# Performance work log

Measured on AMD Instinct MI355X. Metric: run time of the kernel, lower is better.

The kernel has to match this reference:

```python
import jax, jax.numpy as jnp
import numpy as np

N_NODES = 100000
N_EDGES = 1200000
D_IN = 64
D_HID = 64
BN_EPS = 1e-5


def setup_inputs() -> dict:
    key = jax.random.key(0)
    ks = jax.random.split(key, 16)
    x = jax.random.normal(ks[0], (N_NODES, D_IN), dtype=jnp.float32)
    edge_index = jax.random.randint(ks[1], (2, N_EDGES), 0, N_NODES, dtype=jnp.int64)
    s = 1.0 / np.sqrt(D_HID)
    W1 = jax.random.uniform(ks[2], (D_IN, D_HID), jnp.float32, -s, s)
    b1 = jax.random.uniform(ks[3], (D_HID,), jnp.float32, -s, s)
    W2 = jax.random.uniform(ks[4], (D_HID, D_HID), jnp.float32, -s, s)
    b2 = jax.random.uniform(ks[5], (D_HID,), jnp.float32, -s, s)
    W3 = jax.random.uniform(ks[6], (D_HID, D_HID), jnp.float32, -s, s)
    b3 = jax.random.uniform(ks[7], (D_HID,), jnp.float32, -s, s)
    gamma1 = jnp.ones((D_HID,), jnp.float32)
    beta1 = jnp.zeros((D_HID,), jnp.float32)
    gamma2 = jnp.ones((D_HID,), jnp.float32)
    beta2 = jnp.zeros((D_HID,), jnp.float32)
    return {"x": x, "edge_index": edge_index, "batch_size": 1,
            "W1": W1, "b1": b1, "gamma1": gamma1, "beta1": beta1,
            "W2": W2, "b2": b2, "gamma2": gamma2, "beta2": beta2,
            "W3": W3, "b3": b3}


def _gcn_norm(edge_index, n):
    # PyG GCNConv: add self-loops, symmetric normalization D^-1/2 (A+I) D^-1/2
    loop = jnp.arange(n, dtype=edge_index.dtype)
    src = jnp.concatenate([edge_index[0], loop])
    dst = jnp.concatenate([edge_index[1], loop])
    deg = jax.ops.segment_sum(jnp.ones_like(dst, dtype=jnp.float32), dst, num_segments=n)
    dinv = jnp.where(deg > 0, jax.lax.rsqrt(jnp.maximum(deg, 1.0)), 0.0)
    norm = dinv[src] * dinv[dst]  # [E + N]
    return src, dst, norm


def _gcn_conv(h, W, b, src, dst, norm, n):
    h = h @ W                      # [N, D]
    msg = h[src] * norm[:, None]   # gather + scale, [E+N, D]
    out = jax.ops.segment_sum(msg, dst, num_segments=n)  # scatter-add
    return out + b


def _bn_train(h, gamma, beta):
    # BatchNorm1d over nodes, training-mode (biased batch statistics)
    m = h.mean(axis=0)
    v = h.var(axis=0)
    return (h - m) * jax.lax.rsqrt(v + BN_EPS) * gamma + beta


def reference(x, edge_index, batch_size,
              W1, b1, gamma1, beta1, W2, b2, gamma2, beta2, W3, b3):
    n = x.shape[0]
    src, dst, norm = _gcn_norm(edge_index, n)
    h = _gcn_conv(x, W1, b1, src, dst, norm, n)
    h = jax.nn.relu(_bn_train(h, gamma1, beta1))
    h = _gcn_conv(h, W2, b2, src, dst, norm, n)
    h = jax.nn.relu(_bn_train(h, gamma2, beta2))
    h = _gcn_conv(h, W3, b3, src, dst, norm, n)
    return h  # output_type == 'hidden'
```

## Files before the change

### kernel.cpp

```cpp
#include <hip/hip_runtime.h>
#include <hip/hip_bf16.h>

#define D 64

typedef __attribute__((ext_vector_type(8))) short bf16x8;
typedef __attribute__((ext_vector_type(8))) unsigned short u16x8;
typedef __attribute__((ext_vector_type(4))) float f32x4;

__device__ __forceinline__ short f2bf(float x) {
    unsigned u = __float_as_uint(x);
    unsigned r = (u + 0x7fffu + ((u >> 16) & 1u)) >> 16;
    return (short)r;
}
__device__ __forceinline__ float bf2f(unsigned short u) {
    return __uint_as_float((unsigned)u << 16);
}

__global__ void detect_kernel(const unsigned int* e32, int* flag) {
    __shared__ int nz;
    if (threadIdx.x == 0) nz = 0;
    __syncthreads();
    if (e32[2 * threadIdx.x + 1] != 0) nz = 1;
    __syncthreads();
    if (threadIdx.x == 0) *flag = (nz == 0) ? 1 : 0;
}

__device__ __forceinline__ int load_idx(const void* e, int is64, long long i) {
    if (is64) return (int)((const long long*)e)[i];
    return ((const int*)e)[i];
}

#define NBLK 256

__global__ __launch_bounds__(256) void bucket_count_kernel(
    const void* edges, const int* flag, int* pbh, int E, int shift) {
    __shared__ int h[512];
    for (int i = threadIdx.x; i < 512; i += 256) h[i] = 0;
    __syncthreads();
    int is64 = *flag;
    int chunk = (E + gridDim.x - 1) / gridDim.x;
    int s0 = blockIdx.x * chunk;
    int s1 = min(E, s0 + chunk);
    for (int e = s0 + (int)threadIdx.x; e < s1; e += 256) {
        int d = load_idx(edges, is64, (long long)E + e);
        atomicAdd(&h[d >> shift], 1);
    }
    __syncthreads();
    for (int i = threadIdx.x; i < 512; i += 256) pbh[blockIdx.x * 512 + i] = h[i];
}

__global__ __launch_bounds__(256) void colscan_kernel(int* pbh, int* btot) {
    int b = blockIdx.x;
    int k = threadIdx.x;
    __shared__ int sA[256], sB[256];
    int v = pbh[k * 512 + b];
    sA[k] = v;
    __syncthreads();
    int* src = sA;
    int* dst = sB;
    for (int d = 1; d < 256; d <<= 1) {
        dst[k] = src[k] + (k >= d ? src[k - d] : 0);
        __syncthreads();
        int* t = src; src = dst; dst = t;
    }
    pbh[k * 512 + b] = src[k] - v;
    if (k == 255) btot[b] = src[255];
}

__global__ __launch_bounds__(512) void basescan_kernel(const int* btot, int* bbase, int E) {
    __shared__ int sA[512], sB[512];
    int b = threadIdx.x;
    int v = btot[b];
    sA[b] = v;
    __syncthreads();
    int* src = sA;
    int* dst = sB;
    for (int d = 1; d < 512; d <<= 1) {
        dst[b] = src[b] + (b >= d ? src[b - d] : 0);
        __syncthreads();
        int* t = src; src = dst; dst = t;
    }
    bbase[b] = src[b] - v;
    if (b == 0) bbase[512] = E;
}

__global__ __launch_bounds__(256) void bucket_scatter_kernel(
    const void* edges, const int* flag, const int* pbh, const int* bbase,
    unsigned* staging, int E, int shift) {
    __shared__ int cur[512];
    for (int i = threadIdx.x; i < 512; i += 256)
        cur[i] = pbh[blockIdx.x * 512 + i] + bbase[i];
    __syncthreads();
    int is64 = *flag;
    int chunk = (E + gridDim.x - 1) / gridDim.x;
    int s0 = blockIdx.x * chunk;
    int s1 = min(E, s0 + chunk);
    unsigned mask = (unsigned)((1 << shift) - 1);
    for (int e = s0 + (int)threadIdx.x; e < s1; e += 256) {
        int s = load_idx(edges, is64, e);
        int d = load_idx(edges, is64, (long long)E + e);
        int b = d >> shift;
        int pos = atomicAdd(&cur[b], 1);
        staging[pos] = ((unsigned)s << shift) | ((unsigned)d & mask);
    }
}

__global__ __launch_bounds__(256) void bucket_fill_kernel(
    const unsigned* __restrict__ staging, const int* __restrict__ bbase,
    int* __restrict__ offs, float* __restrict__ dinv, int* __restrict__ srcs,
    int shift, int n, int E) {
    int b = blockIdx.x;
    int bstart = bbase[b], bend = bbase[b + 1];
    int bsz = 1 << shift;
    unsigned mask = (unsigned)(bsz - 1);
    int v0 = b << shift;
    int nloc = min(bsz, n - v0);

    __shared__ int cnt[512], cur[512], sA[512], sB[512];
    for (int i = threadIdx.x; i < bsz; i += 256) cnt[i] = 0;
    __syncthreads();
    for (int idx = bstart + (int)threadIdx.x; idx < bend; idx += 256)
        atomicAdd(&cnt[staging[idx] & mask], 1);
    __syncthreads();
    for (int i = threadIdx.x; i < bsz; i += 256) sA[i] = cnt[i];
    __syncthreads();
    int* src = sA;
    int* dst = sB;
    for (int d = 1; d < bsz; d <<= 1) {
        for (int i = threadIdx.x; i < bsz; i += 256)
            dst[i] = src[i] + (i >= d ? src[i - d] : 0);
        __syncthreads();
        int* t = src; src = dst; dst = t;
    }
    for (int i = threadIdx.x; i < bsz; i += 256) {
        int excl = src[i] - cnt[i];
        cur[i] = excl;
        if (i < nloc) {
            offs[v0 + i] = bstart + excl;
            dinv[v0 + i] = rsqrtf((float)(cnt[i] + 1));
        }
    }
    if (b == 0 && threadIdx.x == 0) offs[n] = E;
    __syncthreads();
    for (int idx = bstart + (int)threadIdx.x; idx < bend; idx += 256) {
        unsigned u = staging[idx];
        int ld = (int)(u & mask);
        int pos = atomicAdd(&cur[ld], 1);
        srcs[bstart + pos] = (int)(u >> shift);
    }
}

__global__ __launch_bounds__(256) void mm_bn_kernel(
    const float* __restrict__ Xf, const unsigned short* __restrict__ Xb, int x_is_bf16,
    const float* __restrict__ W,
    const float* __restrict__ slabs, const float* __restrict__ gamma,
    const float* __restrict__ beta, int use_bn, float inv_n,
    const float* __restrict__ dinv,
    unsigned short* __restrict__ Y, int n) {
    int lane = threadIdx.x & 63;
    int m = lane & 15;
    int quad = lane >> 4;

    __shared__ float cn[128];
    if (use_bn) {
        if (threadIdx.x < 128) {
            float s = 0.f;
#pragma unroll
            for (int k = 0; k < 16; k++) s += slabs[k * 128 + (int)threadIdx.x];
            cn[threadIdx.x] = s;
        }
        __syncthreads();
    }

    float sc[16], sh[16];
#pragma unroll
    for (int s = 0; s < 2; s++) {
#pragma unroll
        for (int j = 0; j < 8; j++) {
            float scale = 1.f, shift = 0.f;
            if (use_bn) {
                int f = s * 32 + quad * 8 + j;
                float mean = cn[f] * inv_n;
                float var = cn[64 + f] * inv_n - mean * mean;
                float rs = rsqrtf(var + 1e-5f);
                scale = rs * gamma[f];
                shift = beta[f] - mean * scale;
            }
            sc[s * 8 + j] = scale;
            sh[s * 8 + j] = shift;
        }
    }

    bf16x8 bfrag[4][2];
#pragma unroll
    for (int nt = 0; nt < 4; nt++) {
#pragma unroll
        for (int s = 0; s < 2; s++) {
#pragma unroll
            for (int j = 0; j < 8; j++) {
                int k = s * 32 + quad * 8 + j;
                bfrag[nt][s][j] = f2bf(W[k * 64 + nt * 16 + m]);
            }
        }
    }

    int wave = blockIdx.x * 4 + (threadIdx.x >> 6);
    int nwaves = gridDim.x * 4;
    int ntiles = (n + 15) >> 4;
    const f32x4 zero = {0.f, 0.f, 0.f, 0.f};

    for (int t = wave; t < ntiles; t += nwaves) {
        int r = t * 16 + m;
        if (r >= n) r = n - 1;
        float av[16];
        if (x_is_bf16) {
            const unsigned short* xr = Xb + (long long)r * 64;
            u16x8 u0 = *(const u16x8*)(xr + quad * 8);
            u16x8 u1 = *(const u16x8*)(xr + 32 + quad * 8);
#pragma unroll
            for (int j = 0; j < 8; j++) {
                av[j] = bf2f(u0[j]);
                av[8 + j] = bf2f(u1[j]);
            }
        } else {
            const float* xr = Xf + (long long)r * 64;
            f32x4 a0 = *(const f32x4*)(xr + quad * 8);
            f32x4 a1 = *(const f32x4*)(xr + quad * 8 + 4);
            f32x4 a2 = *(const f32x4*)(xr + 32 + quad * 8);
            f32x4 a3 = *(const f32x4*)(xr + 32 + quad * 8 + 4);
#pragma unroll
            for (int j = 0; j < 4; j++) {
                av[j] = a0[j];
                av[4 + j] = a1[j];
                av[8 + j] = a2[j];
                av[12 + j] = a3[j];
            }
        }
        bf16x8 A0, A1;
#pragma unroll
        for (int j = 0; j < 8; j++) {
            float v0 = av[j] * sc[j] + sh[j];
            float v1 = av[8 + j] * sc[8 + j] + sh[8 + j];
            if (use_bn) {
                v0 = fmaxf(v0, 0.f);
                v1 = fmaxf(v1, 0.f);
            }
            A0[j] = f2bf(v0);
            A1[j] = f2bf(v1);
        }

        f32x4 acc[4];
#pragma unroll
        for (int nt = 0; nt < 4; nt++) {
            acc[nt] = __builtin_amdgcn_mfma_f32_16x16x32_bf16(A0, bfrag[nt][0], zero, 0, 0, 0);
            acc[nt] = __builtin_amdgcn_mfma_f32_16x16x32_bf16(A1, bfrag[nt][1], acc[nt], 0, 0, 0);
        }

        int row0 = t * 16 + quad * 4;
        float dv[4];
#pragma unroll
        for (int i = 0; i < 4; i++) {
            int rr = row0 + i;
            dv[i] = (rr < n) ? dinv[rr] : 0.f;
        }
#pragma unroll
        for (int nt = 0; nt < 4; nt++) {
#pragma unroll
            for (int i = 0; i < 4; i++) {
                int rr = row0 + i;
                if (rr < n)
                    Y[(long long)rr * 64 + nt * 16 + m] = (unsigned short)f2bf(acc[nt][i] * dv[i]);
            }
        }
    }
}

__global__ __launch_bounds__(256) void agg_kernel(const unsigned short* __restrict__ T,
                                                  const int* __restrict__ offs,
                                                  const int* __restrict__ srcs,
                                                  const float* __restrict__ dinv,
                                                  const float* __restrict__ bias,
                                                  unsigned short* __restrict__ out16,
                                                  float* __restrict__ out32, int out_bf16,
                                                  float* __restrict__ slabs, int do_stats,
                                                  int n) {
    int v = blockIdx.x * 4 + (threadIdx.x >> 6);
    int lane = threadIdx.x & 63;
    int valid = v < n;
    int vc = valid ? v : n - 1;
    float val;
    {
        float acc = bf2f(T[((unsigned)vc << 6) + lane]);
        int j0 = __builtin_amdgcn_readfirstlane(offs[vc]);
        int j1 = __builtin_amdgcn_readfirstlane(offs[vc + 1]);
        for (int j = j0; j < j1; j += 16) {
            int sidx[16];
#pragma unroll
            for (int u = 0; u < 16; u++) {
                int jj = j + u;
                int s = srcs[jj];
                sidx[u] = (jj < j1) ? s : n;
            }
            float t[16];
#pragma unroll
            for (int u = 0; u < 16; u++)
                t[u] = bf2f(T[((unsigned)sidx[u] << 6) + lane]);
            float p0 = (t[0] + t[1]) + (t[2] + t[3]);
            float p1 = (t[4] + t[5]) + (t[6] + t[7]);
            float p2 = (t[8] + t[9]) + (t[10] + t[11]);
            float p3 = (t[12] + t[13]) + (t[14] + t[15]);
            acc += (p0 + p1) + (p2 + p3);
        }
        val = dinv[vc] * acc + bias[lane];
        if (valid) {
            if (out_bf16)
                out16[((unsigned)v << 6) + lane] = (unsigned short)f2bf(val);
            else
                out32[((unsigned)v << 6) + lane] = val;
        }
    }
    if (do_stats) {
        __shared__ float ls[256], lq[256];
        float x = valid ? val : 0.f;
        ls[threadIdx.x] = x;
        lq[threadIdx.x] = x * x;
        __syncthreads();
        int tid = threadIdx.x;
        if (tid < 128) {
            int f = tid & 63;
            const float* a = (tid < 64) ? ls : lq;
            float r = a[f] + a[64 + f] + a[128 + f] + a[192 + f];
            atomicAdd(&slabs[((unsigned)(blockIdx.x & 15)) * 128 + tid], r);
        }
    }
}

extern "C" void kernel_launch(void* const* d_in, const int* in_sizes, int n_in,
                              void* d_out, int out_size, void* d_ws, size_t ws_size,
                              hipStream_t stream) {
    const float* x = (const float*)d_in[0];
    const void* edges = d_in[1];
    const float* W1 = (const float*)d_in[3];
    const float* b1 = (const float*)d_in[4];
    const float* gamma1 = (const float*)d_in[5];
    const float* beta1 = (const float*)d_in[6];
    const float* W2 = (const float*)d_in[7];
    const float* b2 = (const float*)d_in[8];
    const float* gamma2 = (const float*)d_in[9];
    const float* beta2 = (const float*)d_in[10];
    const float* W3 = (const float*)d_in[11];
    const float* b3 = (const float*)d_in[12];

    const int N = in_sizes[0] / D;
    const int E = in_sizes[1] / 2;
    const float inv_n = 1.f / (float)N;

    int shift = 8;
    while ((((long long)N - 1) >> shift) + 1 > 512) shift++;
    const int nbuk = (int)(((long long)N - 1) >> shift) + 1;

    char* ws = (char*)d_ws;
    size_t off = 0;
    auto alloc = [&](size_t bytes) -> void* {
        void* p = ws + off;
        off = (off + bytes + 255) & ~(size_t)255;
        return p;
    };
    float*    dinv    = (float*)   alloc((size_t)N * 4);
    int*      offs    = (int*)     alloc((size_t)(N + 1) * 4);
    int*      srcs    = (int*)     alloc(((size_t)E + 16) * 4);
    unsigned* staging = (unsigned*)alloc((size_t)E * 4);
    int*      pbh     = (int*)     alloc((size_t)NBLK * 512 * 4);
    int*      btot    = (int*)     alloc(512 * 4);
    int*      bbase   = (int*)     alloc(513 * 4);
    int*      flag    = (int*)     alloc(4);
    float*    slabs   = (float*)   alloc((size_t)2 * 16 * 128 * 4);
    unsigned short* bufA = (unsigned short*)alloc((size_t)(N + 1) * D * 2);
    unsigned short* hbuf = (unsigned short*)alloc((size_t)N * D * 2);
    float*    outf    = (float*)d_out;

    const int AGGB = (N + 3) / 4;
    const int MMB  = 782;

    detect_kernel<<<1, 256, 0, stream>>>((const unsigned int*)edges, flag);
    bucket_count_kernel<<<NBLK, 256, 0, stream>>>(edges, flag, pbh, E, shift);
    colscan_kernel<<<512, 256, 0, stream>>>(pbh, btot);
    basescan_kernel<<<1, 512, 0, stream>>>(btot, bbase, E);
    bucket_scatter_kernel<<<NBLK, 256, 0, stream>>>(edges, flag, pbh, bbase, staging, E, shift);
    bucket_fill_kernel<<<nbuk, 256, 0, stream>>>(staging, bbase, offs, dinv, srcs, shift, N, E);
    hipMemsetAsync(slabs, 0, (size_t)2 * 16 * 128 * 4, stream);
    hipMemsetAsync(bufA + (size_t)N * D, 0, D * 2, stream);

    mm_bn_kernel<<<MMB, 256, 0, stream>>>(x, nullptr, 0, W1, nullptr, nullptr, nullptr, 0,
                                          inv_n, dinv, bufA, N);
    agg_kernel<<<AGGB, 256, 0, stream>>>(bufA, offs, srcs, dinv, b1, hbuf, nullptr, 1,
                                         slabs, 1, N);

    mm_bn_kernel<<<MMB, 256, 0, stream>>>(nullptr, hbuf, 1, W2, slabs, gamma1, beta1, 1,
                                          inv_n, dinv, bufA, N);
    agg_kernel<<<AGGB, 256, 0, stream>>>(bufA, offs, srcs, dinv, b2, hbuf, nullptr, 1,
                                         slabs + 16 * 128, 1, N);

    mm_bn_kernel<<<MMB, 256, 0, stream>>>(nullptr, hbuf, 1, W3, slabs + 16 * 128, gamma2, beta2, 1,
                                          inv_n, dinv, bufA, N);
    agg_kernel<<<AGGB, 256, 0, stream>>>(bufA, offs, srcs, dinv, b3, nullptr, outf, 0,
                                         nullptr, 0, N);
}
```

Measured before the change: 306.6 us.

## Fold detect and memsets into kernels, coalesce mm output via LDS, resize grid

Removes the separate detect kernel and two memset launches by detecting 64-bit edge indices inside each bucket kernel and zeroing the stats slabs and padding row from existing kernels. The matmul epilogue now stages bf16 results in shared memory and writes each row with 16-byte vector stores instead of scattered 2-byte stores. The matmul grid is sized to one tile per wave rather than a fixed block count. This trades a few extra global reads per block for fewer launches and better-coalesced writes.

New measurement: 299.8 us. 2.2% less time.

```diff
diff --git a/kernel.cpp b/kernel.cpp
--- a/kernel.cpp
+++ b/kernel.cpp
@@ -16,13 +16,13 @@
     return __uint_as_float((unsigned)u << 16);
 }
 
-__global__ void detect_kernel(const unsigned int* e32, int* flag) {
+__device__ __forceinline__ int block_detect_is64(const unsigned* e32) {
     __shared__ int nz;
     if (threadIdx.x == 0) nz = 0;
     __syncthreads();
-    if (e32[2 * threadIdx.x + 1] != 0) nz = 1;
-    __syncthreads();
-    if (threadIdx.x == 0) *flag = (nz == 0) ? 1 : 0;
+    if (threadIdx.x < 256 && e32[2 * threadIdx.x + 1] != 0) nz = 1;
+    __syncthreads();
+    return nz == 0;
 }
 
 __device__ __forceinline__ int load_idx(const void* e, int is64, long long i) {
@@ -33,11 +33,13 @@
 #define NBLK 256
 
 __global__ __launch_bounds__(256) void bucket_count_kernel(
-    const void* edges, const int* flag, int* pbh, int E, int shift) {
+    const void* edges, int* pbh, float* slabs, int E, int shift) {
+    int is64 = block_detect_is64((const unsigned*)edges);
+    if (blockIdx.x == 0)
+        for (int i = threadIdx.x; i < 2 * 16 * 128; i += 256) slabs[i] = 0.f;
     __shared__ int h[512];
     for (int i = threadIdx.x; i < 512; i += 256) h[i] = 0;
     __syncthreads();
-    int is64 = *flag;
     int chunk = (E + gridDim.x - 1) / gridDim.x;
     int s0 = blockIdx.x * chunk;
     int s1 = min(E, s0 + chunk);
@@ -85,13 +87,13 @@
 }
 
 __global__ __launch_bounds__(256) void bucket_scatter_kernel(
-    const void* edges, const int* flag, const int* pbh, const int* bbase,
+    const void* edges, const int* pbh, const int* bbase,
     unsigned* staging, int E, int shift) {
+    int is64 = block_detect_is64((const unsigned*)edges);
     __shared__ int cur[512];
     for (int i = threadIdx.x; i < 512; i += 256)
         cur[i] = pbh[blockIdx.x * 512 + i] + bbase[i];
     __syncthreads();
-    int is64 = *flag;
     int chunk = (E + gridDim.x - 1) / gridDim.x;
     int s0 = blockIdx.x * chunk;
     int s1 = min(E, s0 + chunk);
@@ -108,8 +110,9 @@
 __global__ __launch_bounds__(256) void bucket_fill_kernel(
     const unsigned* __restrict__ staging, const int* __restrict__ bbase,
     int* __restrict__ offs, float* __restrict__ dinv, int* __restrict__ srcs,
-    int shift, int n, int E) {
+    unsigned short* __restrict__ zrow, int shift, int n, int E) {
     int b = blockIdx.x;
+    if (b == 0 && threadIdx.x < 64) zrow[threadIdx.x] = 0;
     int bstart = bbase[b], bend = bbase[b + 1];
     int bsz = 1 << shift;
     unsigned mask = (unsigned)(bsz - 1);
@@ -160,8 +163,11 @@
     int lane = threadIdx.x & 63;
     int m = lane & 15;
     int quad = lane >> 4;
+    int w = threadIdx.x >> 6;
 
     __shared__ float cn[128];
+    __shared__ __align__(16) unsigned short ty[4][16][72];
+
     if (use_bn) {
         if (threadIdx.x < 128) {
             float s = 0.f;
@@ -204,7 +210,7 @@
         }
     }
 
-    int wave = blockIdx.x * 4 + (threadIdx.x >> 6);
+    int wave = blockIdx.x * 4 + w;
     int nwaves = gridDim.x * 4;
     int ntiles = (n + 15) >> 4;
     const f32x4 zero = {0.f, 0.f, 0.f, 0.f};
@@ -257,20 +263,26 @@
         }
 
         int row0 = t * 16 + quad * 4;
-        float dv[4];
+        float dvv[4];
 #pragma unroll
         for (int i = 0; i < 4; i++) {
             int rr = row0 + i;
-            dv[i] = (rr < n) ? dinv[rr] : 0.f;
+            dvv[i] = (rr < n) ? dinv[rr] : 0.f;
         }
 #pragma unroll
         for (int nt = 0; nt < 4; nt++) {
 #pragma unroll
-            for (int i = 0; i < 4; i++) {
-                int rr = row0 + i;
-                if (rr < n)
-                    Y[(long long)rr * 64 + nt * 16 + m] = (unsigned short)f2bf(acc[nt][i] * dv[i]);
-            }
+            for (int i = 0; i < 4; i++)
+                ty[w][quad * 4 + i][nt * 16 + m] =
+                    (unsigned short)f2bf(acc[nt][i] * dvv[i]);
+        }
+        int lr = lane >> 2, lc = lane & 3;
+        u16x8 o0 = *(const u16x8*)&ty[w][lr][lc * 16];
+        u16x8 o1 = *(const u16x8*)&ty[w][lr][lc * 16 + 8];
+        int rr = t * 16 + lr;
+        if (rr < n) {
+            *(u16x8*)(Y + ((unsigned)rr << 6) + lc * 16) = o0;
+            *(u16x8*)(Y + ((unsigned)rr << 6) + lc * 16 + 8) = o1;
         }
     }
 }
@@ -373,23 +385,20 @@
     int*      pbh     = (int*)     alloc((size_t)NBLK * 512 * 4);
     int*      btot    = (int*)     alloc(512 * 4);
     int*      bbase   = (int*)     alloc(513 * 4);
-    int*      flag    = (int*)     alloc(4);
     float*    slabs   = (float*)   alloc((size_t)2 * 16 * 128 * 4);
     unsigned short* bufA = (unsigned short*)alloc((size_t)(N + 1) * D * 2);
     unsigned short* hbuf = (unsigned short*)alloc((size_t)N * D * 2);
     float*    outf    = (float*)d_out;
 
     const int AGGB = (N + 3) / 4;
-    const int MMB  = 782;
-
-    detect_kernel<<<1, 256, 0, stream>>>((const unsigned int*)edges, flag);
-    bucket_count_kernel<<<NBLK, 256, 0, stream>>>(edges, flag, pbh, E, shift);
+    const int MMB  = (((N + 15) >> 4) + 3) / 4;
+
+    bucket_count_kernel<<<NBLK, 256, 0, stream>>>(edges, pbh, slabs, E, shift);
     colscan_kernel<<<512, 256, 0, stream>>>(pbh, btot);
     basescan_kernel<<<1, 512, 0, stream>>>(btot, bbase, E);
-    bucket_scatter_kernel<<<NBLK, 256, 0, stream>>>(edges, flag, pbh, bbase, staging, E, shift);
-    bucket_fill_kernel<<<nbuk, 256, 0, stream>>>(staging, bbase, offs, dinv, srcs, shift, N, E);
-    hipMemsetAsync(slabs, 0, (size_t)2 * 16 * 128 * 4, stream);
-    hipMemsetAsync(bufA + (size_t)N * D, 0, D * 2, stream);
+    bucket_scatter_kernel<<<NBLK, 256, 0, stream>>>(edges, pbh, bbase, staging, E, shift);
+    bucket_fill_kernel<<<nbuk, 256, 0, stream>>>(staging, bbase, offs, dinv, srcs,
+                                                 bufA + (size_t)N * D, shift, N, E);
 
     mm_bn_kernel<<<MMB, 256, 0, stream>>>(x, nullptr, 0, W1, nullptr, nullptr, nullptr, 0,
                                           inv_n, dinv, bufA, N);
```
